# Optimization experiments

Measured on AMD Instinct MI355X. Metric: run time of the kernel, lower is better.

The kernel has to match this reference:

```python
import jax, jax.numpy as jnp
import numpy as np

N_NODES = 50000
N_EDGES = 800000
F_DIM = 64
NEG_SLOPE_ATT = 0.2   # GATConv attention LeakyReLU
NEG_SLOPE_ACT = 0.01  # nn.LeakyReLU default between layers


def setup_inputs() -> dict:
    key = jax.random.key(0)
    ks = jax.random.split(key, 10)
    s = 1.0 / np.sqrt(F_DIM)
    return {
        "x": jax.random.normal(ks[0], (N_NODES, F_DIM), jnp.float32),
        "edge_index": jax.random.randint(ks[1], (2, N_EDGES), 0, N_NODES, jnp.int64),
        "W0": jax.random.normal(ks[2], (F_DIM, F_DIM), jnp.float32) * s,
        "a_src0": jax.random.normal(ks[3], (F_DIM,), jnp.float32) * s,
        "a_dst0": jax.random.normal(ks[4], (F_DIM,), jnp.float32) * s,
        "b0": jnp.zeros((F_DIM,), jnp.float32),
        "W1": jax.random.normal(ks[5], (F_DIM, F_DIM), jnp.float32) * s,
        "a_src1": jax.random.normal(ks[6], (F_DIM,), jnp.float32) * s,
        "a_dst1": jax.random.normal(ks[7], (F_DIM,), jnp.float32) * s,
        "b1": jnp.zeros((F_DIM,), jnp.float32),
    }


def _gat_layer(x, src, dst, W, a_src, a_dst, b, n_nodes):
    # x: [N,F]; src/dst: [E'] (self-loops included)
    h = x @ W                                   # [N,F]
    alpha_s = h @ a_src                          # [N]
    alpha_d = h @ a_dst                          # [N]
    e = jax.nn.leaky_relu(alpha_s[src] + alpha_d[dst], NEG_SLOPE_ATT)  # [E']
    # scatter-softmax over incoming edges per destination node
    m = jax.ops.segment_max(e, dst, num_segments=n_nodes)              # [N]
    ex = jnp.exp(e - m[dst])                                           # [E']
    z = jax.ops.segment_sum(ex, dst, num_segments=n_nodes)             # [N]
    alpha = ex / (z[dst] + 1e-16)                                      # [E']
    out = jax.ops.segment_sum(h[src] * alpha[:, None], dst, num_segments=n_nodes)
    return out + b


def reference(x, edge_index, W0, a_src0, a_dst0, b0, W1, a_src1, a_dst1, b1):
    n = x.shape[0]
    loops = jnp.arange(n, dtype=edge_index.dtype)
    src = jnp.concatenate([edge_index[0], loops])  # add_self_loops=True
    dst = jnp.concatenate([edge_index[1], loops])
    h = _gat_layer(x, src, dst, W0, a_src0, a_dst0, b0, n)
    h = jax.nn.leaky_relu(h, NEG_SLOPE_ACT)
    h = _gat_layer(h, src, dst, W1, a_src1, a_dst1, b1, n)
    h = jax.nn.leaky_relu(h, NEG_SLOPE_ACT)
    return h + x  # residual with original input features
```

## Files before the change

### kernel.cpp

```cpp
#include <hip/hip_runtime.h>
#include <math.h>

#define NNODES 50000
#define NEDGES 800000
#define ETOT   850000
#define F      64
#define NB     782
#define CAP    1408
#define LIN_BLOCKS 1563
#define AGG_BLOCKS 1563
#define SBLK   256
#define SIT    13
#define SEPB   (256 * SIT)
#define XSP    68

typedef unsigned short u16;
typedef unsigned int   u32;

__device__ __forceinline__ u32 f2bf2(float a, float b) {
    u32 ua = __float_as_uint(a), ub = __float_as_uint(b);
    ua = (ua + 0x7FFFu + ((ua >> 16) & 1u)) >> 16;
    ub = (ub + 0x7FFFu + ((ub >> 16) & 1u)) >> 16;
    return ua | (ub << 16);
}

#define ACC8(ev, hv) \
    a0 = fmaf(ev, __uint_as_float(hv.x << 16),         a0); \
    a1 = fmaf(ev, __uint_as_float(hv.x & 0xFFFF0000u), a1); \
    a2 = fmaf(ev, __uint_as_float(hv.y << 16),         a2); \
    a3 = fmaf(ev, __uint_as_float(hv.y & 0xFFFF0000u), a3); \
    a4 = fmaf(ev, __uint_as_float(hv.z << 16),         a4); \
    a5 = fmaf(ev, __uint_as_float(hv.z & 0xFFFF0000u), a5); \
    a6 = fmaf(ev, __uint_as_float(hv.w << 16),         a6); \
    a7 = fmaf(ev, __uint_as_float(hv.w & 0xFFFF0000u), a7)

struct LinSmem {
    float Ws[F * F];
    float xs[32 * XSP];
    float asv[F], adv[F];
};

__device__ __forceinline__ void linear_body(
    LinSmem& sm,
    const float* __restrict__ x, const float* __restrict__ W,
    const float* __restrict__ a_src, const float* __restrict__ a_dst,
    u16* __restrict__ h16, float* __restrict__ as_, float* __restrict__ ad_,
    int blk)
{
    const int tid = threadIdx.x;
    const int n   = tid >> 3;
    const int c0  = (tid & 7) * 8;
    const int node = blk * 32 + n;
    const bool valid = node < NNODES;

    for (int i = tid * 4; i < F * F; i += 1024)
        *(float4*)&sm.Ws[i] = *(const float4*)&W[i];
    if (tid < F) { sm.asv[tid] = a_src[tid]; sm.adv[tid] = a_dst[tid]; }
    if (valid) {
        const float4 v0 = *(const float4*)&x[(size_t)node * F + c0];
        const float4 v1 = *(const float4*)&x[(size_t)node * F + c0 + 4];
        *(float4*)&sm.xs[n * XSP + c0]     = v0;
        *(float4*)&sm.xs[n * XSP + c0 + 4] = v1;
    }
    __syncthreads();

    float o0=0.f,o1=0.f,o2=0.f,o3=0.f,o4=0.f,o5=0.f,o6=0.f,o7=0.f;
#pragma unroll 8
    for (int k = 0; k < F; ++k) {
        const float xv = sm.xs[n * XSP + k];
        const float4 wa = *(const float4*)&sm.Ws[k * F + c0];
        const float4 wb = *(const float4*)&sm.Ws[k * F + c0 + 4];
        o0 = fmaf(xv, wa.x, o0); o1 = fmaf(xv, wa.y, o1);
        o2 = fmaf(xv, wa.z, o2); o3 = fmaf(xv, wa.w, o3);
        o4 = fmaf(xv, wb.x, o4); o5 = fmaf(xv, wb.y, o5);
        o6 = fmaf(xv, wb.z, o6); o7 = fmaf(xv, wb.w, o7);
    }

    float vs = o0*sm.asv[c0]   + o1*sm.asv[c0+1] + o2*sm.asv[c0+2] + o3*sm.asv[c0+3]
             + o4*sm.asv[c0+4] + o5*sm.asv[c0+5] + o6*sm.asv[c0+6] + o7*sm.asv[c0+7];
    float vd = o0*sm.adv[c0]   + o1*sm.adv[c0+1] + o2*sm.adv[c0+2] + o3*sm.adv[c0+3]
             + o4*sm.adv[c0+4] + o5*sm.adv[c0+5] + o6*sm.adv[c0+6] + o7*sm.adv[c0+7];
    vs += __shfl_xor(vs, 1, 64); vs += __shfl_xor(vs, 2, 64); vs += __shfl_xor(vs, 4, 64);
    vd += __shfl_xor(vd, 1, 64); vd += __shfl_xor(vd, 2, 64); vd += __shfl_xor(vd, 4, 64);

    if (valid) {
        if ((tid & 7) == 0) { as_[node] = vs; ad_[node] = vd; }
        uint4 p;
        p.x = f2bf2(o0, o1); p.y = f2bf2(o2, o3);
        p.z = f2bf2(o4, o5); p.w = f2bf2(o6, o7);
        *(uint4*)&h16[(size_t)node * F + c0] = p;
    }
}

__global__ __launch_bounds__(256) void stage_linear1(
    const float* __restrict__ x, const float* __restrict__ W,
    const float* __restrict__ a_src, const float* __restrict__ a_dst,
    u16* __restrict__ h16, float* __restrict__ as_, float* __restrict__ ad_,
    const int* __restrict__ src, const int* __restrict__ dst,
    int* __restrict__ gcur, u32* __restrict__ stg)
{
    __shared__ LinSmem sm;
    if (blockIdx.x < SBLK) {
        int* cnt  = (int*)&sm;
        int* lcur = cnt + NB;
        for (int i = threadIdx.x; i < NB; i += 256) cnt[i] = 0;
        __syncthreads();
        const int base = blockIdx.x * SEPB;
        int es[SIT], ed[SIT];
#pragma unroll
        for (int it = 0; it < SIT; ++it) {
            const int e = base + it * 256 + threadIdx.x;
            if (e < ETOT) {
                int s, d;
                if (e < NEDGES) { s = src[e]; d = dst[e]; }
                else            { s = e - NEDGES; d = s; }
                es[it] = s; ed[it] = d;
                atomicAdd(&cnt[d >> 6], 1);
            } else {
                ed[it] = -1; es[it] = 0;
            }
        }
        __syncthreads();
        for (int i = threadIdx.x; i < NB; i += 256)
            lcur[i] = cnt[i] ? (i * CAP + atomicAdd(&gcur[i], cnt[i])) : 0;
        __syncthreads();
#pragma unroll
        for (int it = 0; it < SIT; ++it) {
            if (ed[it] >= 0) {
                const int p = atomicAdd(&lcur[ed[it] >> 6], 1);
                stg[p] = ((u32)(ed[it] & 63) << 16) | (u32)es[it];
            }
        }
        return;
    }
    linear_body(sm, x, W, a_src, a_dst, h16, as_, ad_, blockIdx.x - SBLK);
}

__global__ __launch_bounds__(256) void bucket_csr(
    const int* __restrict__ gcur, const u32* __restrict__ stg,
    u16* __restrict__ csr, int* __restrict__ rowptr, int* __restrict__ rowcnt)
{
    __shared__ int cnt[64];
    const int b = blockIdx.x;
    const int nbase = b << 6;
    const int nr  = (NNODES - nbase < 64) ? (NNODES - nbase) : 64;
    const int beg = b * CAP;
    const int m   = gcur[b];

    if (threadIdx.x < 64) cnt[threadIdx.x] = 0;
    __syncthreads();
    for (int i = threadIdx.x; i < m; i += 256)
        atomicAdd(&cnt[stg[beg + i] >> 16], 1);
    __syncthreads();
    if (threadIdx.x < 64) {
        const int v = cnt[threadIdx.x];
        int incl = v;
#pragma unroll
        for (int off = 1; off < 64; off <<= 1) {
            const int t = __shfl_up(incl, off, 64);
            if (threadIdx.x >= off) incl += t;
        }
        const int pos = beg + incl - v;
        cnt[threadIdx.x] = pos;
        if (threadIdx.x < nr) {
            rowptr[nbase + threadIdx.x] = pos;
            rowcnt[nbase + threadIdx.x] = v;
        }
    }
    __syncthreads();
    for (int i = threadIdx.x; i < m; i += 256) {
        const u32 pk = stg[beg + i];
        const int pos = atomicAdd(&cnt[pk >> 16], 1);
        csr[pos] = (u16)(pk & 0xFFFFu);
    }
}

template<int MODE>
__global__ __launch_bounds__(256) void gat_agg(
    const int* __restrict__ rowptr, const int* __restrict__ rowcnt,
    const u16* __restrict__ csr, const u16* __restrict__ hin,
    const float* __restrict__ as_, const float* __restrict__ ad_,
    const float* __restrict__ bias,
    const float* __restrict__ Wn, const float* __restrict__ an_s,
    const float* __restrict__ an_d,
    u16* __restrict__ hout, float* __restrict__ as_out, float* __restrict__ ad_out,
    const float* __restrict__ resid, float* __restrict__ out)
{
    __shared__ float Ws[MODE == 0 ? F * F : 1];
    __shared__ float asv[MODE == 0 ? F : 1], adv[MODE == 0 ? F : 1];
    __shared__ float xs[MODE == 0 ? 32 * XSP : 1];

    const int tid = threadIdx.x;
    const int ln  = tid & 63;
    const int g   = ln >> 3;
    const int l   = ln & 7;
    const int nb  = (tid >> 6) * 8 + g;
    const int node = blockIdx.x * 32 + nb;
    const bool valid = node < NNODES;

    if constexpr (MODE == 0) {
        for (int i = tid * 4; i < F * F; i += 1024)
            *(float4*)&Ws[i] = *(const float4*)&Wn[i];
        if (tid < F) { asv[tid] = an_s[tid]; adv[tid] = an_d[tid]; }
    }

    int beg = 0, cnt = 0;
    float ad_n = 0.f;
    if (valid) {
        beg  = rowptr[node];
        cnt  = rowcnt[node];
        ad_n = ad_[node];
    }

    float a0=0.f,a1=0.f,a2=0.f,a3=0.f,a4=0.f,a5=0.f,a6=0.f,a7=0.f;
    float z = 0.f;
    const int nfull = cnt & ~3;
    int i = 0;
    for (; i < nfull; i += 4) {
        const int s1 = csr[beg + i];
        const int s2 = csr[beg + i + 1];
        const int s3 = csr[beg + i + 2];
        const int s4 = csr[beg + i + 3];
        const float r1 = as_[s1] + ad_n;
        const float r2 = as_[s2] + ad_n;
        const float r3 = as_[s3] + ad_n;
        const float r4 = as_[s4] + ad_n;
        const uint4 h1 = ((const uint4*)(hin + (size_t)s1 * F))[l];
        const uint4 h2 = ((const uint4*)(hin + (size_t)s2 * F))[l];
        const uint4 h3 = ((const uint4*)(hin + (size_t)s3 * F))[l];
        const uint4 h4 = ((const uint4*)(hin + (size_t)s4 * F))[l];
        const float t1 = (r1 > 0.f) ? r1 : 0.2f * r1;
        const float t2 = (r2 > 0.f) ? r2 : 0.2f * r2;
        const float t3 = (r3 > 0.f) ? r3 : 0.2f * r3;
        const float t4 = (r4 > 0.f) ? r4 : 0.2f * r4;
        const float e1 = __expf(t1);
        const float e2 = __expf(t2);
        const float e3 = __expf(t3);
        const float e4 = __expf(t4);
        z += (e1 + e2) + (e3 + e4);
        ACC8(e1, h1); ACC8(e2, h2); ACC8(e3, h3); ACC8(e4, h4);
    }
    if (i < cnt) {
        const int j2 = (i + 1 < cnt) ? (i + 1) : i;
        const int j3 = (i + 2 < cnt) ? (i + 2) : i;
        const int s1 = csr[beg + i];
        const int s2 = csr[beg + j2];
        const int s3 = csr[beg + j3];
        const float r1 = as_[s1] + ad_n;
        const float r2 = as_[s2] + ad_n;
        const float r3 = as_[s3] + ad_n;
        const uint4 h1 = ((const uint4*)(hin + (size_t)s1 * F))[l];
        const uint4 h2 = ((const uint4*)(hin + (size_t)s2 * F))[l];
        const uint4 h3 = ((const uint4*)(hin + (size_t)s3 * F))[l];
        const float t1 = (r1 > 0.f) ? r1 : 0.2f * r1;
        const float t2 = (r2 > 0.f) ? r2 : 0.2f * r2;
        const float t3 = (r3 > 0.f) ? r3 : 0.2f * r3;
        const float e1 = __expf(t1);
        const float e2 = (i + 1 < cnt) ? __expf(t2) : 0.f;
        const float e3 = (i + 2 < cnt) ? __expf(t3) : 0.f;
        z += e1 + e2 + e3;
        ACC8(e1, h1); ACC8(e2, h2); ACC8(e3, h3);
    }

    const float inv = 1.f / (z + 1e-16f);
    const float4 b0v = *(const float4*)&bias[l * 8];
    const float4 b1v = *(const float4*)&bias[l * 8 + 4];
    float v0 = a0 * inv + b0v.x, v1 = a1 * inv + b0v.y;
    float v2 = a2 * inv + b0v.z, v3 = a3 * inv + b0v.w;
    float v4 = a4 * inv + b1v.x, v5 = a5 * inv + b1v.y;
    float v6 = a6 * inv + b1v.z, v7 = a7 * inv + b1v.w;
    v0 = (v0 > 0.f) ? v0 : 0.01f * v0;  v1 = (v1 > 0.f) ? v1 : 0.01f * v1;
    v2 = (v2 > 0.f) ? v2 : 0.01f * v2;  v3 = (v3 > 0.f) ? v3 : 0.01f * v3;
    v4 = (v4 > 0.f) ? v4 : 0.01f * v4;  v5 = (v5 > 0.f) ? v5 : 0.01f * v5;
    v6 = (v6 > 0.f) ? v6 : 0.01f * v6;  v7 = (v7 > 0.f) ? v7 : 0.01f * v7;

    if constexpr (MODE == 0) {
        {
            float4 w0; w0.x = v0; w0.y = v1; w0.z = v2; w0.w = v3;
            float4 w1; w1.x = v4; w1.y = v5; w1.z = v6; w1.w = v7;
            const int xb = nb * XSP + l * 8;
            *(float4*)&xs[xb]     = w0;
            *(float4*)&xs[xb + 4] = w1;
        }
        __syncthreads();

        const int nb2 = tid >> 3;
        const int c0  = (tid & 7) * 8;
        float o0=0.f,o1=0.f,o2=0.f,o3=0.f,o4=0.f,o5=0.f,o6=0.f,o7=0.f;
#pragma unroll 8
        for (int k = 0; k < F; ++k) {
            const float xv = xs[nb2 * XSP + k];
            const float4 wa = *(const float4*)&Ws[k * F + c0];
            const float4 wb = *(const float4*)&Ws[k * F + c0 + 4];
            o0 = fmaf(xv, wa.x, o0); o1 = fmaf(xv, wa.y, o1);
            o2 = fmaf(xv, wa.z, o2); o3 = fmaf(xv, wa.w, o3);
            o4 = fmaf(xv, wb.x, o4); o5 = fmaf(xv, wb.y, o5);
            o6 = fmaf(xv, wb.z, o6); o7 = fmaf(xv, wb.w, o7);
        }
        const int node2 = blockIdx.x * 32 + nb2;
        float vs = o0*asv[c0]   + o1*asv[c0+1] + o2*asv[c0+2] + o3*asv[c0+3]
                 + o4*asv[c0+4] + o5*asv[c0+5] + o6*asv[c0+6] + o7*asv[c0+7];
        float vd = o0*adv[c0]   + o1*adv[c0+1] + o2*adv[c0+2] + o3*adv[c0+3]
                 + o4*adv[c0+4] + o5*adv[c0+5] + o6*adv[c0+6] + o7*adv[c0+7];
        vs += __shfl_xor(vs, 1, 64); vs += __shfl_xor(vs, 2, 64); vs += __shfl_xor(vs, 4, 64);
        vd += __shfl_xor(vd, 1, 64); vd += __shfl_xor(vd, 2, 64); vd += __shfl_xor(vd, 4, 64);
        if (node2 < NNODES) {
            if ((tid & 7) == 0) { as_out[node2] = vs; ad_out[node2] = vd; }
            uint4 p;
            p.x = f2bf2(o0, o1); p.y = f2bf2(o2, o3);
            p.z = f2bf2(o4, o5); p.w = f2bf2(o6, o7);
            *(uint4*)&hout[(size_t)node2 * F + c0] = p;
        }
    } else {
        if (valid) {
            const float4 r0 = *(const float4*)(resid + (size_t)node * F + l * 8);
            const float4 r1 = *(const float4*)(resid + (size_t)node * F + l * 8 + 4);
            float4 o0, o1;
            o0.x = v0 + r0.x; o0.y = v1 + r0.y; o0.z = v2 + r0.z; o0.w = v3 + r0.w;
            o1.x = v4 + r1.x; o1.y = v5 + r1.y; o1.z = v6 + r1.z; o1.w = v7 + r1.w;
            *(float4*)(out + (size_t)node * F + l * 8)     = o0;
            *(float4*)(out + (size_t)node * F + l * 8 + 4) = o1;
        }
    }
}

extern "C" void kernel_launch(void* const* d_in, const int* in_sizes, int n_in,
                              void* d_out, int out_size, void* d_ws, size_t ws_size,
                              hipStream_t stream)
{
    const float* x   = (const float*)d_in[0];
    const int*   ei  = (const int*)  d_in[1];
    const float* W0  = (const float*)d_in[2];
    const float* as0 = (const float*)d_in[3];
    const float* ad0 = (const float*)d_in[4];
    const float* b0  = (const float*)d_in[5];
    const float* W1  = (const float*)d_in[6];
    const float* as1 = (const float*)d_in[7];
    const float* ad1 = (const float*)d_in[8];
    const float* b1  = (const float*)d_in[9];
    float* out = (float*)d_out;

    const int* src = ei;
    const int* dst = ei + NEDGES;

    char* ws = (char*)d_ws;
    u16*   h16    = (u16*)ws;   ws += (size_t)NNODES * F * 2;
    u16*   h2_16  = (u16*)ws;   ws += (size_t)NNODES * F * 2;
    float* as_    = (float*)ws; ws += (size_t)NNODES * 4;
    float* ad_    = (float*)ws; ws += (size_t)NNODES * 4;
    float* as2    = (float*)ws; ws += (size_t)NNODES * 4;
    float* ad2    = (float*)ws; ws += (size_t)NNODES * 4;
    int*   rowptr = (int*)ws;   ws += (size_t)NNODES * 4;
    int*   rowcnt = (int*)ws;   ws += (size_t)NNODES * 4;
    int*   gcur   = (int*)ws;   ws += (size_t)NB * 4;
    u32*   stg    = (u32*)ws;   ws += (size_t)NB * CAP * 4;
    u16*   csr    = (u16*)ws;   ws += (size_t)NB * CAP * 2;

    hipMemsetAsync(gcur, 0, (size_t)NB * 4, stream);
    stage_linear1<<<SBLK + LIN_BLOCKS, 256, 0, stream>>>(
        x, W0, as0, ad0, h16, as_, ad_, src, dst, gcur, stg);
    bucket_csr<<<NB, 256, 0, stream>>>(gcur, stg, csr, rowptr, rowcnt);

    gat_agg<0><<<AGG_BLOCKS, 256, 0, stream>>>(
        rowptr, rowcnt, csr, h16, as_, ad_, b0,
        W1, as1, ad1, h2_16, as2, ad2, nullptr, nullptr);
    gat_agg<1><<<AGG_BLOCKS, 256, 0, stream>>>(
        rowptr, rowcnt, csr, h2_16, as2, ad2, b1,
        nullptr, nullptr, nullptr, nullptr, nullptr, nullptr, x, out);
}
```

Measured before the change: 170.4 us.

## Fuse bucket CSR build into aggregation kernels with shared-memory edge lists

Drops the separate bucket_csr kernel. Each aggregation block (now 512 threads, one bucket of 64 nodes) counts and scans its staged edges in shared memory and builds the per-node edge list there. It also precomputes each edge's exp(leakyrelu) attention weight once, stored as fp16 next to the source index. This removes a launch and the global csr/rowptr/rowcnt traffic, and takes the per-edge exp out of the inner gather loop, at the cost of repeating the bucket sort in both layers and rounding attention weights to fp16.

```diff
diff --git a/kernel.cpp b/kernel.cpp
--- a/kernel.cpp
+++ b/kernel.cpp
@@ -1,4 +1,5 @@
 #include <hip/hip_runtime.h>
+#include <hip/hip_fp16.h>
 #include <math.h>
 
 #define NNODES 50000
@@ -8,7 +9,6 @@
 #define NB     782
 #define CAP    1408
 #define LIN_BLOCKS 1563
-#define AGG_BLOCKS 1563
 #define SBLK   256
 #define SIT    13
 #define SEPB   (256 * SIT)
@@ -136,49 +136,10 @@
     linear_body(sm, x, W, a_src, a_dst, h16, as_, ad_, blockIdx.x - SBLK);
 }
 
-__global__ __launch_bounds__(256) void bucket_csr(
+template<int MODE>
+__global__ __launch_bounds__(512) void gat_agg(
     const int* __restrict__ gcur, const u32* __restrict__ stg,
-    u16* __restrict__ csr, int* __restrict__ rowptr, int* __restrict__ rowcnt)
-{
-    __shared__ int cnt[64];
-    const int b = blockIdx.x;
-    const int nbase = b << 6;
-    const int nr  = (NNODES - nbase < 64) ? (NNODES - nbase) : 64;
-    const int beg = b * CAP;
-    const int m   = gcur[b];
-
-    if (threadIdx.x < 64) cnt[threadIdx.x] = 0;
-    __syncthreads();
-    for (int i = threadIdx.x; i < m; i += 256)
-        atomicAdd(&cnt[stg[beg + i] >> 16], 1);
-    __syncthreads();
-    if (threadIdx.x < 64) {
-        const int v = cnt[threadIdx.x];
-        int incl = v;
-#pragma unroll
-        for (int off = 1; off < 64; off <<= 1) {
-            const int t = __shfl_up(incl, off, 64);
-            if (threadIdx.x >= off) incl += t;
-        }
-        const int pos = beg + incl - v;
-        cnt[threadIdx.x] = pos;
-        if (threadIdx.x < nr) {
-            rowptr[nbase + threadIdx.x] = pos;
-            rowcnt[nbase + threadIdx.x] = v;
-        }
-    }
-    __syncthreads();
-    for (int i = threadIdx.x; i < m; i += 256) {
-        const u32 pk = stg[beg + i];
-        const int pos = atomicAdd(&cnt[pk >> 16], 1);
-        csr[pos] = (u16)(pk & 0xFFFFu);
-    }
-}
-
-template<int MODE>
-__global__ __launch_bounds__(256) void gat_agg(
-    const int* __restrict__ rowptr, const int* __restrict__ rowcnt,
-    const u16* __restrict__ csr, const u16* __restrict__ hin,
+    const u16* __restrict__ hin,
     const float* __restrict__ as_, const float* __restrict__ ad_,
     const float* __restrict__ bias,
     const float* __restrict__ Wn, const float* __restrict__ an_s,
@@ -186,78 +147,95 @@
     u16* __restrict__ hout, float* __restrict__ as_out, float* __restrict__ ad_out,
     const float* __restrict__ resid, float* __restrict__ out)
 {
+    __shared__ u32  csrE[CAP];
+    __shared__ int  cnt[64];
+    __shared__ int  rp[64];
+    __shared__ float advn[64];
     __shared__ float Ws[MODE == 0 ? F * F : 1];
     __shared__ float asv[MODE == 0 ? F : 1], adv[MODE == 0 ? F : 1];
-    __shared__ float xs[MODE == 0 ? 32 * XSP : 1];
-
-    const int tid = threadIdx.x;
-    const int ln  = tid & 63;
-    const int g   = ln >> 3;
-    const int l   = ln & 7;
-    const int nb  = (tid >> 6) * 8 + g;
-    const int node = blockIdx.x * 32 + nb;
-    const bool valid = node < NNODES;
-
+    __shared__ float xs[MODE == 0 ? 64 * XSP : 1];
+
+    const int tid   = threadIdx.x;
+    const int b     = blockIdx.x;
+    const int nbase = b << 6;
+    const int nr    = (NNODES - nbase < 64) ? (NNODES - nbase) : 64;
+    const int m     = gcur[b];
+
+    if (tid < 64) {
+        cnt[tid]  = 0;
+        advn[tid] = (tid < nr) ? ad_[nbase + tid] : 0.f;
+    }
     if constexpr (MODE == 0) {
-        for (int i = tid * 4; i < F * F; i += 1024)
+        for (int i = tid * 4; i < F * F; i += 2048)
             *(float4*)&Ws[i] = *(const float4*)&Wn[i];
         if (tid < F) { asv[tid] = an_s[tid]; adv[tid] = an_d[tid]; }
     }
-
-    int beg = 0, cnt = 0;
-    float ad_n = 0.f;
-    if (valid) {
-        beg  = rowptr[node];
-        cnt  = rowcnt[node];
-        ad_n = ad_[node];
-    }
+    __syncthreads();
+
+    for (int i = tid; i < m; i += 512)
+        atomicAdd(&cnt[stg[b * CAP + i] >> 16], 1);
+    __syncthreads();
+    if (tid < 64) {
+        const int v = cnt[tid];
+        int incl = v;
+#pragma unroll
+        for (int off = 1; off < 64; off <<= 1) {
+            const int t = __shfl_up(incl, off, 64);
+            if (tid >= off) incl += t;
+        }
+        rp[tid]  = incl - v;
+        cnt[tid] = incl - v;
+    }
+    __syncthreads();
+    for (int i = tid; i < m; i += 512) {
+        const u32 pk = stg[b * CAP + i];
+        const int d6 = pk >> 16;
+        const int s  = pk & 0xFFFFu;
+        float r = as_[s] + advn[d6];
+        r = (r > 0.f) ? r : 0.2f * r;
+        const float ev = __expf(r);
+        const int pos = atomicAdd(&cnt[d6], 1);
+        csrE[pos] = ((u32)__half_as_ushort(__float2half(ev)) << 16) | (u32)s;
+    }
+    __syncthreads();
+
+    const int n   = tid >> 3;
+    const int l   = tid & 7;
+    const int beg = rp[n];
+    const int deg = cnt[n] - rp[n];
 
     float a0=0.f,a1=0.f,a2=0.f,a3=0.f,a4=0.f,a5=0.f,a6=0.f,a7=0.f;
     float z = 0.f;
-    const int nfull = cnt & ~3;
+    const int nfull = deg & ~3;
     int i = 0;
     for (; i < nfull; i += 4) {
-        const int s1 = csr[beg + i];
-        const int s2 = csr[beg + i + 1];
-        const int s3 = csr[beg + i + 2];
-        const int s4 = csr[beg + i + 3];
-        const float r1 = as_[s1] + ad_n;
-        const float r2 = as_[s2] + ad_n;
-        const float r3 = as_[s3] + ad_n;
-        const float r4 = as_[s4] + ad_n;
-        const uint4 h1 = ((const uint4*)(hin + (size_t)s1 * F))[l];
-        const uint4 h2 = ((const uint4*)(hin + (size_t)s2 * F))[l];
-        const uint4 h3 = ((const uint4*)(hin + (size_t)s3 * F))[l];
-        const uint4 h4 = ((const uint4*)(hin + (size_t)s4 * F))[l];
-        const float t1 = (r1 > 0.f) ? r1 : 0.2f * r1;
-        const float t2 = (r2 > 0.f) ? r2 : 0.2f * r2;
-        const float t3 = (r3 > 0.f) ? r3 : 0.2f * r3;
-        const float t4 = (r4 > 0.f) ? r4 : 0.2f * r4;
-        const float e1 = __expf(t1);
-        const float e2 = __expf(t2);
-        const float e3 = __expf(t3);
-        const float e4 = __expf(t4);
+        const u32 p1 = csrE[beg + i];
+        const u32 p2 = csrE[beg + i + 1];
+        const u32 p3 = csrE[beg + i + 2];
+        const u32 p4 = csrE[beg + i + 3];
+        const uint4 h1 = ((const uint4*)(hin + (size_t)(p1 & 0xFFFFu) * F))[l];
+        const uint4 h2 = ((const uint4*)(hin + (size_t)(p2 & 0xFFFFu) * F))[l];
+        const uint4 h3 = ((const uint4*)(hin + (size_t)(p3 & 0xFFFFu) * F))[l];
+        const uint4 h4 = ((const uint4*)(hin + (size_t)(p4 & 0xFFFFu) * F))[l];
+        const float e1 = __half2float(__ushort_as_half((u16)(p1 >> 16)));
+        const float e2 = __half2float(__ushort_as_half((u16)(p2 >> 16)));
+        const float e3 = __half2float(__ushort_as_half((u16)(p3 >> 16)));
+        const float e4 = __half2float(__ushort_as_half((u16)(p4 >> 16)));
         z += (e1 + e2) + (e3 + e4);
         ACC8(e1, h1); ACC8(e2, h2); ACC8(e3, h3); ACC8(e4, h4);
     }
-    if (i < cnt) {
-        const int j2 = (i + 1 < cnt) ? (i + 1) : i;
-        const int j3 = (i + 2 < cnt) ? (i + 2) : i;
-        const int s1 = csr[beg + i];
-        const int s2 = csr[beg + j2];
-        const int s3 = csr[beg + j3];
-        const float r1 = as_[s1] + ad_n;
-        const float r2 = as_[s2] + ad_n;
-        const float r3 = as_[s3] + ad_n;
-        const uint4 h1 = ((const uint4*)(hin + (size_t)s1 * F))[l];
-        const uint4 h2 = ((const uint4*)(hin + (size_t)s2 * F))[l];
-        const uint4 h3 = ((const uint4*)(hin + (size_t)s3 * F))[l];
-        const float t1 = (r1 > 0.f) ? r1 : 0.2f * r1;
-        const float t2 = (r2 > 0.f) ? r2 : 0.2f * r2;
-        const float t3 = (r3 > 0.f) ? r3 : 0.2f * r3;
-        const float e1 = __expf(t1);
-        const float e2 = (i + 1 < cnt) ? __expf(t2) : 0.f;
-        const float e3 = (i + 2 < cnt) ? __expf(t3) : 0.f;
+    if (i < deg) {
+        const int j2 = (i + 1 < deg) ? (i + 1) : i;
+        const int j3 = (i + 2 < deg) ? (i + 2) : i;
+        const u32 p1 = csrE[beg + i];
+        const u32 p2 = csrE[beg + j2];
+        const u32 p3 = csrE[beg + j3];
+        const uint4 h1 = ((const uint4*)(hin + (size_t)(p1 & 0xFFFFu) * F))[l];
+        const uint4 h2 = ((const uint4*)(hin + (size_t)(p2 & 0xFFFFu) * F))[l];
+        const uint4 h3 = ((const uint4*)(hin + (size_t)(p3 & 0xFFFFu) * F))[l];
+        const float e1 = __half2float(__ushort_as_half((u16)(p1 >> 16)));
+        const float e2 = (i + 1 < deg) ? __half2float(__ushort_as_half((u16)(p2 >> 16))) : 0.f;
+        const float e3 = (i + 2 < deg) ? __half2float(__ushort_as_half((u16)(p3 >> 16))) : 0.f;
         z += e1 + e2 + e3;
         ACC8(e1, h1); ACC8(e2, h2); ACC8(e3, h3);
     }
@@ -278,7 +256,7 @@
         {
             float4 w0; w0.x = v0; w0.y = v1; w0.z = v2; w0.w = v3;
             float4 w1; w1.x = v4; w1.y = v5; w1.z = v6; w1.w = v7;
-            const int xb = nb * XSP + l * 8;
+            const int xb = n * XSP + l * 8;
             *(float4*)&xs[xb]     = w0;
             *(float4*)&xs[xb + 4] = w1;
         }
@@ -297,14 +275,14 @@
             o4 = fmaf(xv, wb.x, o4); o5 = fmaf(xv, wb.y, o5);
             o6 = fmaf(xv, wb.z, o6); o7 = fmaf(xv, wb.w, o7);
         }
-        const int node2 = blockIdx.x * 32 + nb2;
         float vs = o0*asv[c0]   + o1*asv[c0+1] + o2*asv[c0+2] + o3*asv[c0+3]
                  + o4*asv[c0+4] + o5*asv[c0+5] + o6*asv[c0+6] + o7*asv[c0+7];
         float vd = o0*adv[c0]   + o1*adv[c0+1] + o2*adv[c0+2] + o3*adv[c0+3]
                  + o4*adv[c0+4] + o5*adv[c0+5] + o6*adv[c0+6] + o7*adv[c0+7];
         vs += __shfl_xor(vs, 1, 64); vs += __shfl_xor(vs, 2, 64); vs += __shfl_xor(vs, 4, 64);
         vd += __shfl_xor(vd, 1, 64); vd += __shfl_xor(vd, 2, 64); vd += __shfl_xor(vd, 4, 64);
-        if (node2 < NNODES) {
+        if (nb2 < nr) {
+            const int node2 = nbase + nb2;
             if ((tid & 7) == 0) { as_out[node2] = vs; ad_out[node2] = vd; }
             uint4 p;
             p.x = f2bf2(o0, o1); p.y = f2bf2(o2, o3);
@@ -312,7 +290,8 @@
             *(uint4*)&hout[(size_t)node2 * F + c0] = p;
         }
     } else {
-        if (valid) {
+        if (n < nr) {
+            const int node = nbase + n;
             const float4 r0 = *(const float4*)(resid + (size_t)node * F + l * 8);
             const float4 r1 = *(const float4*)(resid + (size_t)node * F + l * 8 + 4);
             float4 o0, o1;
@@ -350,21 +329,17 @@
     float* ad_    = (float*)ws; ws += (size_t)NNODES * 4;
     float* as2    = (float*)ws; ws += (size_t)NNODES * 4;
     float* ad2    = (float*)ws; ws += (size_t)NNODES * 4;
-    int*   rowptr = (int*)ws;   ws += (size_t)NNODES * 4;
-    int*   rowcnt = (int*)ws;   ws += (size_t)NNODES * 4;
     int*   gcur   = (int*)ws;   ws += (size_t)NB * 4;
     u32*   stg    = (u32*)ws;   ws += (size_t)NB * CAP * 4;
-    u16*   csr    = (u16*)ws;   ws += (size_t)NB * CAP * 2;
 
     hipMemsetAsync(gcur, 0, (size_t)NB * 4, stream);
     stage_linear1<<<SBLK + LIN_BLOCKS, 256, 0, stream>>>(
         x, W0, as0, ad0, h16, as_, ad_, src, dst, gcur, stg);
-    bucket_csr<<<NB, 256, 0, stream>>>(gcur, stg, csr, rowptr, rowcnt);
-
-    gat_agg<0><<<AGG_BLOCKS, 256, 0, stream>>>(
-        rowptr, rowcnt, csr, h16, as_, ad_, b0,
+
+    gat_agg<0><<<NB, 512, 0, stream>>>(
+        gcur, stg, h16, as_, ad_, b0,
         W1, as1, ad1, h2_16, as2, ad2, nullptr, nullptr);
-    gat_agg<1><<<AGG_BLOCKS, 256, 0, stream>>>(
-        rowptr, rowcnt, csr, h2_16, as2, ad2, b1,
+    gat_agg<1><<<NB, 512, 0, stream>>>(
+        gcur, stg, h2_16, as2, ad2, b1,
         nullptr, nullptr, nullptr, nullptr, nullptr, nullptr, x, out);
 }
```

Measured after the change: 166.6 us. 1.02x faster.
